# Kernel tuning notes

Measured on AMD Instinct MI355X. Metric: run time of the kernel, lower is better.

The kernel has to match this reference:

```python
import jax, jax.numpy as jnp
import numpy as np

INPUT_SIZE, HIDDEN, OUT = 2, 32, 1

def setup_inputs() -> dict:
    key = jax.random.key(0)
    ks = jax.random.split(key, 8)
    B, T = 2048, 512
    s_ih = 1.0 / np.sqrt(HIDDEN)
    return {
        "x": jax.random.normal(ks[0], (B, T, INPUT_SIZE), dtype=jnp.float32),
        "W_ih": jax.random.uniform(ks[1], (4 * HIDDEN, INPUT_SIZE), minval=-s_ih, maxval=s_ih, dtype=jnp.float32),
        "W_hh": jax.random.uniform(ks[2], (4 * HIDDEN, HIDDEN), minval=-s_ih, maxval=s_ih, dtype=jnp.float32),
        "b_ih": jax.random.uniform(ks[3], (4 * HIDDEN,), minval=-s_ih, maxval=s_ih, dtype=jnp.float32),
        "b_hh": jax.random.uniform(ks[4], (4 * HIDDEN,), minval=-s_ih, maxval=s_ih, dtype=jnp.float32),
        "W_fc": jax.random.uniform(ks[5], (OUT, HIDDEN), minval=-s_ih, maxval=s_ih, dtype=jnp.float32),
        "b_fc": jax.random.uniform(ks[6], (OUT,), minval=-s_ih, maxval=s_ih, dtype=jnp.float32),
    }

def _lstm(x, W_ih, W_hh, b_ih, b_hh):
    # x: [B, T, I]; PyTorch gate order: i, f, g, o
    B, T, _ = x.shape
    H = W_hh.shape[1]
    # precompute input projections for all timesteps: [T, B, 4H]
    xp = jnp.einsum('bti,gi->tbg', x, W_ih) + (b_ih + b_hh)

    def step(carry, xp_t):
        h, c = carry
        gates = xp_t + h @ W_hh.T  # [B, 4H]
        i, f, g, o = jnp.split(gates, 4, axis=-1)
        i = jax.nn.sigmoid(i)
        f = jax.nn.sigmoid(f)
        g = jnp.tanh(g)
        o = jax.nn.sigmoid(o)
        c = f * c + i * g
        h = o * jnp.tanh(c)
        return (h, c), h

    h0 = jnp.zeros((B, H), dtype=x.dtype)
    c0 = jnp.zeros((B, H), dtype=x.dtype)
    _, hs = jax.lax.scan(step, (h0, c0), xp)  # hs: [T, B, H]
    return jnp.transpose(hs, (1, 0, 2))  # [B, T, H]

def reference(x, W_ih, W_hh, b_ih, b_hh, W_fc, b_fc):
    lstm_out = _lstm(x, W_ih, W_hh, b_ih, b_hh)  # [B, T, H]
    return lstm_out @ W_fc.T + b_fc  # [B, T, OUT]
```

## Files before the change

### kernel.cpp

```cpp
#include <hip/hip_runtime.h>


#define BB 2048
#define TT 512
#define HH 32
#define CHUNK 32
#define ROWH 40
#define WSH (2 * CHUNK * ROWH + 8)

#define LOG2E 1.44269504088896340736f

typedef float v2f __attribute__((ext_vector_type(2)));
typedef float v4f __attribute__((ext_vector_type(4)));
typedef unsigned int v4u __attribute__((ext_vector_type(4)));
typedef _Float16 h2 __attribute__((ext_vector_type(2)));

__device__ __forceinline__ float sigm2(float xs) {
    return __builtin_amdgcn_rcpf(1.0f + __builtin_amdgcn_exp2f(-xs));
}

__device__ __forceinline__ h2 u2h(unsigned int u) {
    return __builtin_bit_cast(h2, u);
}

#if defined(__has_builtin)
#if __has_builtin(__builtin_amdgcn_fdot2)
#define FDOT2(a, b, c) __builtin_amdgcn_fdot2((a), (b), (c), false)
#endif
#endif
#ifndef FDOT2
#define FDOT2(a, b, c) fmaf((float)(a).y, (float)(b).y, \
                            fmaf((float)(a).x, (float)(b).x, (c)))
#endif

__global__ __launch_bounds__(256, 1) void lstm_fused_kernel(
    const float* __restrict__ x,
    const float* __restrict__ W_ih,
    const float* __restrict__ W_hh,
    const float* __restrict__ b_ih,
    const float* __restrict__ b_hh,
    const float* __restrict__ W_fc,
    const float* __restrict__ b_fc,
    float* __restrict__ out)
{
    __shared__ __align__(16) _Float16 lds_h[4][WSH];

    const int lane = threadIdx.x & 63;
    const int wv   = threadIdx.x >> 6;
    const int j    = lane & 31;
    const bool low = (lane < 32);
    const int b    = blockIdx.x * 8 + wv * 2 + (low ? 0 : 1);

    const int ri = j, rf = HH + j, rg = 2 * HH + j, ro = 3 * HH + j;
    const float si = LOG2E;
    const float sg = 2.0f * LOG2E;

    const v2f wihI = ((const v2f*)W_ih)[ri] * si;
    const v2f wihF = ((const v2f*)W_ih)[rf] * si;
    const v2f wihG = ((const v2f*)W_ih)[rg] * sg;
    const v2f wihO = ((const v2f*)W_ih)[ro] * si;
    const float bI = (b_ih[ri] + b_hh[ri]) * si;
    const float bF = (b_ih[rf] + b_hh[rf]) * si;
    const float bG = (b_ih[rg] + b_hh[rg]) * sg;
    const float bO = (b_ih[ro] + b_hh[ro]) * si;

    h2 wI[16], wF[16], wG[16], wO[16];
    #pragma unroll
    for (int k = 0; k < 16; ++k) {
        v2f a;
        a = ((const v2f*)(W_hh + ri * HH))[k] * si;
        wI[k] = (h2){(_Float16)a.x, (_Float16)a.y};
        a = ((const v2f*)(W_hh + rf * HH))[k] * si;
        wF[k] = (h2){(_Float16)a.x, (_Float16)a.y};
        a = ((const v2f*)(W_hh + rg * HH))[k] * sg;
        wG[k] = (h2){(_Float16)a.x, (_Float16)a.y};
        a = ((const v2f*)(W_hh + ro * HH))[k] * si;
        wO[k] = (h2){(_Float16)a.x, (_Float16)a.y};
    }

    h2 wfc2[16];
    #pragma unroll
    for (int k = 0; k < 16; ++k) {
        v2f a = ((const v2f*)W_fc)[k];
        wfc2[k] = (h2){(_Float16)a.x, (_Float16)a.y};
    }
    const float bfc = b_fc[0];

    float c = 0.0f;

    _Float16* hb = &lds_h[wv][low ? 0 : CHUNK * ROWH];
    _Float16* wr = hb + j;

    hb[(CHUNK - 1) * ROWH + j] = (_Float16)0.0f;

    v4u hq[4];
    {
        const v4u* rq = (const v4u*)(hb + (CHUNK - 1) * ROWH);
        #pragma unroll
        for (int q = 0; q < 4; ++q) hq[q] = rq[q];
    }

    const float* xb = x + (size_t)b * (TT * 2);
    float* outp = out + (size_t)b * TT + j;

    v4f xq0 = *(const v4f*)(xb);
    v4f xq1 = *(const v4f*)(xb + 4);

    #pragma unroll 1
    for (int ch = 0; ch < TT / CHUNK; ++ch) {
        #pragma unroll 1
        for (int uu = 0; uu < CHUNK; uu += 4) {
            const int t = ch * CHUNK + uu;
            const float* xnx = (t + 4 < TT) ? (xb + (t + 4) * 2) : xb;
            v4f nxq0 = *(const v4f*)(xnx);
            v4f nxq1 = *(const v4f*)(xnx + 4);

            #pragma unroll
            for (int s = 0; s < 4; ++s) {
                v2f xt;
                if      (s == 0) xt = (v2f){xq0.x, xq0.y};
                else if (s == 1) xt = (v2f){xq0.z, xq0.w};
                else if (s == 2) xt = (v2f){xq1.x, xq1.y};
                else             xt = (v2f){xq1.z, xq1.w};

                float aI0 = fmaf(xt.y, wihI.y, fmaf(xt.x, wihI.x, bI));
                float aF0 = fmaf(xt.y, wihF.y, fmaf(xt.x, wihF.x, bF));
                float aG0 = fmaf(xt.y, wihG.y, fmaf(xt.x, wihG.x, bG));
                float aO0 = fmaf(xt.y, wihO.y, fmaf(xt.x, wihO.x, bO));
                float aI1, aF1, aG1, aO1;

                #pragma unroll
                for (int k = 0; k < 16; ++k) {
                    h2 hp = u2h(hq[k >> 2][k & 3]);
                    if (k < 8) {
                        aI0 = FDOT2(hp, wI[k], aI0);
                        aF0 = FDOT2(hp, wF[k], aF0);
                        aG0 = FDOT2(hp, wG[k], aG0);
                        aO0 = FDOT2(hp, wO[k], aO0);
                    } else if (k == 8) {
                        aI1 = FDOT2(hp, wI[k], 0.0f);
                        aF1 = FDOT2(hp, wF[k], 0.0f);
                        aG1 = FDOT2(hp, wG[k], 0.0f);
                        aO1 = FDOT2(hp, wO[k], 0.0f);
                    } else {
                        aI1 = FDOT2(hp, wI[k], aI1);
                        aF1 = FDOT2(hp, wF[k], aF1);
                        aG1 = FDOT2(hp, wG[k], aG1);
                        aO1 = FDOT2(hp, wO[k], aO1);
                    }
                }
                float gi = aI0 + aI1;
                float gf = aF0 + aF1;
                float gg = aG0 + aG1;
                float go = aO0 + aO1;

                float iv = sigm2(gi);
                float fv = sigm2(gf);
                float ov = sigm2(go);
                float gv = fmaf(4.0f * LOG2E, sigm2(gg), -2.0f * LOG2E);

                c = fmaf(fv, c, iv * gv);

                float rr   = sigm2(c);
                float hnew = fmaf(ov + ov, rr, -ov);

                *wr = (_Float16)hnew;
                {
                    const v4u* rq = (const v4u*)(wr - j);
                    #pragma unroll
                    for (int q = 0; q < 4; ++q) hq[q] = rq[q];
                }
                wr += ROWH;
            }
            xq0 = nxq0; xq1 = nxq1;
        }

        wr -= CHUNK * ROWH;

        {
            const v4u* fr = (const v4u*)(hb + j * ROWH);
            v4u f[4];
            #pragma unroll
            for (int q = 0; q < 4; ++q) f[q] = fr[q];
            float acc = bfc;
            #pragma unroll
            for (int k = 0; k < 16; ++k)
                acc = FDOT2(u2h(f[k >> 2][k & 3]), wfc2[k], acc);
            *outp = acc;
            outp += CHUNK;
        }
    }
}

extern "C" void kernel_launch(void* const* d_in, const int* in_sizes, int n_in,
                              void* d_out, int out_size, void* d_ws, size_t ws_size,
                              hipStream_t stream) {
    const float* x    = (const float*)d_in[0];
    const float* W_ih = (const float*)d_in[1];
    const float* W_hh = (const float*)d_in[2];
    const float* b_ih = (const float*)d_in[3];
    const float* b_hh = (const float*)d_in[4];
    const float* W_fc = (const float*)d_in[5];
    const float* b_fc = (const float*)d_in[6];
    float* out = (float*)d_out;

    dim3 grid(BB / 8);
    dim3 block(256);
    lstm_fused_kernel<<<grid, block, 0, stream>>>(x, W_ih, W_hh, b_ih, b_hh,
                                                  W_fc, b_fc, out);
}
```

Measured before the change: 194.1 us.

## Exchange hidden state via permlane32 swap and DPP rotations instead of LDS

Replaces the per-step LDS write and 64-byte readback of the hidden vector with an in-register exchange. A permlane32_swap pairs the two halves, then a tree of DPP row rotations builds all 16 packed h pairs. W_hh weights are permuted to match the rotated lane order through an LDS-staged copy, and the FC head now reads fp32 h rows with a padded stride. This takes LDS latency off the serial recurrence, at the cost of about 15 dependent DPP moves per step and more setup work.

```diff
diff --git a/kernel.cpp b/kernel.cpp
--- a/kernel.cpp
+++ b/kernel.cpp
@@ -5,14 +5,13 @@
 #define TT 512
 #define HH 32
 #define CHUNK 32
-#define ROWH 40
-#define WSH (2 * CHUNK * ROWH + 8)
+#define ROWF 33
 
 #define LOG2E 1.44269504088896340736f
 
 typedef float v2f __attribute__((ext_vector_type(2)));
 typedef float v4f __attribute__((ext_vector_type(4)));
-typedef unsigned int v4u __attribute__((ext_vector_type(4)));
+typedef unsigned int v2u __attribute__((ext_vector_type(2)));
 typedef _Float16 h2 __attribute__((ext_vector_type(2)));
 
 __device__ __forceinline__ float sigm2(float xs) {
@@ -32,6 +31,9 @@
 #define FDOT2(a, b, c) fmaf((float)(a).y, (float)(b).y, \
                             fmaf((float)(a).x, (float)(b).x, (c)))
 #endif
+
+#define DPP_ROR(src, amt) \
+    ((unsigned)__builtin_amdgcn_mov_dpp((int)(src), 0x120 | (amt), 0xf, 0xf, true))
 
 __global__ __launch_bounds__(256, 1) void lstm_fused_kernel(
     const float* __restrict__ x,
@@ -43,17 +45,74 @@
     const float* __restrict__ b_fc,
     float* __restrict__ out)
 {
-    __shared__ __align__(16) _Float16 lds_h[4][WSH];
+    __shared__ float lds_w[128 * HH];
+    __shared__ __align__(16) float lds_h[4][2 * CHUNK * ROWF];
 
     const int lane = threadIdx.x & 63;
     const int wv   = threadIdx.x >> 6;
-    const int j    = lane & 31;
-    const bool low = (lane < 32);
-    const int b    = blockIdx.x * 8 + wv * 2 + (low ? 0 : 1);
+    const bool lo32 = (lane < 32);
+    const int elem = (lane >> 4) & 1;
+    const int j    = (lane & 15) | ((lane >> 1) & 16);
+    const int b    = blockIdx.x * 8 + wv * 2 + elem;
+
+    {
+        const v4f* src = (const v4f*)W_hh;
+        v4f* dst = (v4f*)lds_w;
+        #pragma unroll
+        for (int r = 0; r < (128 * HH / 4) / 256; ++r)
+            dst[r * 256 + threadIdx.x] = src[r * 256 + threadIdx.x];
+    }
+    __syncthreads();
+
+    unsigned P[16];
+    auto exch = [&](float hn) {
+        v2u r = __builtin_amdgcn_permlane32_swap(
+            __float_as_uint(hn), __float_as_uint(hn), false, false);
+        float hx = __uint_as_float(lo32 ? r.y : r.x);
+        h2 pk = {(_Float16)hn, (_Float16)hx};
+        P[0] = __builtin_bit_cast(unsigned, pk);
+        P[1] = DPP_ROR(P[0], 1);
+        P[2] = DPP_ROR(P[0], 2);
+        P[3] = DPP_ROR(P[1], 2);
+        P[4] = DPP_ROR(P[0], 4);
+        P[5] = DPP_ROR(P[1], 4);
+        P[6] = DPP_ROR(P[2], 4);
+        P[7] = DPP_ROR(P[3], 4);
+        P[8]  = DPP_ROR(P[0], 8);
+        P[9]  = DPP_ROR(P[1], 8);
+        P[10] = DPP_ROR(P[2], 8);
+        P[11] = DPP_ROR(P[3], 8);
+        P[12] = DPP_ROR(P[4], 8);
+        P[13] = DPP_ROR(P[5], 8);
+        P[14] = DPP_ROR(P[6], 8);
+        P[15] = DPP_ROR(P[7], 8);
+    };
+
+    exch((float)j);
+    int klo[16], khi[16];
+    #pragma unroll
+    for (int m = 0; m < 16; ++m) {
+        h2 hp = u2h(P[m]);
+        klo[m] = (int)(float)hp.x;
+        khi[m] = (int)(float)hp.y;
+    }
 
     const int ri = j, rf = HH + j, rg = 2 * HH + j, ro = 3 * HH + j;
     const float si = LOG2E;
     const float sg = 2.0f * LOG2E;
+
+    h2 wIp[16], wFp[16], wGp[16], wOp[16];
+    #pragma unroll
+    for (int m = 0; m < 16; ++m) {
+        wIp[m] = (h2){(_Float16)(lds_w[ri * HH + klo[m]] * si),
+                      (_Float16)(lds_w[ri * HH + khi[m]] * si)};
+        wFp[m] = (h2){(_Float16)(lds_w[rf * HH + klo[m]] * si),
+                      (_Float16)(lds_w[rf * HH + khi[m]] * si)};
+        wGp[m] = (h2){(_Float16)(lds_w[rg * HH + klo[m]] * sg),
+                      (_Float16)(lds_w[rg * HH + khi[m]] * sg)};
+        wOp[m] = (h2){(_Float16)(lds_w[ro * HH + klo[m]] * si),
+                      (_Float16)(lds_w[ro * HH + khi[m]] * si)};
+    }
 
     const v2f wihI = ((const v2f*)W_ih)[ri] * si;
     const v2f wihF = ((const v2f*)W_ih)[rf] * si;
@@ -64,41 +123,18 @@
     const float bG = (b_ih[rg] + b_hh[rg]) * sg;
     const float bO = (b_ih[ro] + b_hh[ro]) * si;
 
-    h2 wI[16], wF[16], wG[16], wO[16];
-    #pragma unroll
-    for (int k = 0; k < 16; ++k) {
-        v2f a;
-        a = ((const v2f*)(W_hh + ri * HH))[k] * si;
-        wI[k] = (h2){(_Float16)a.x, (_Float16)a.y};
-        a = ((const v2f*)(W_hh + rf * HH))[k] * si;
-        wF[k] = (h2){(_Float16)a.x, (_Float16)a.y};
-        a = ((const v2f*)(W_hh + rg * HH))[k] * sg;
-        wG[k] = (h2){(_Float16)a.x, (_Float16)a.y};
-        a = ((const v2f*)(W_hh + ro * HH))[k] * si;
-        wO[k] = (h2){(_Float16)a.x, (_Float16)a.y};
-    }
-
-    h2 wfc2[16];
-    #pragma unroll
-    for (int k = 0; k < 16; ++k) {
-        v2f a = ((const v2f*)W_fc)[k];
-        wfc2[k] = (h2){(_Float16)a.x, (_Float16)a.y};
-    }
+    float wfc[HH];
+    #pragma unroll
+    for (int u = 0; u < HH; ++u) wfc[u] = W_fc[u];
     const float bfc = b_fc[0];
 
     float c = 0.0f;
 
-    _Float16* hb = &lds_h[wv][low ? 0 : CHUNK * ROWH];
-    _Float16* wr = hb + j;
-
-    hb[(CHUNK - 1) * ROWH + j] = (_Float16)0.0f;
-
-    v4u hq[4];
-    {
-        const v4u* rq = (const v4u*)(hb + (CHUNK - 1) * ROWH);
-        #pragma unroll
-        for (int q = 0; q < 4; ++q) hq[q] = rq[q];
-    }
+    float* hbE = &lds_h[wv][elem * CHUNK * ROWF];
+    float* wr  = hbE + j;
+
+    #pragma unroll
+    for (int m = 0; m < 16; ++m) P[m] = 0u;
 
     const float* xb = x + (size_t)b * (TT * 2);
     float* outp = out + (size_t)b * TT + j;
@@ -131,22 +167,22 @@
 
                 #pragma unroll
                 for (int k = 0; k < 16; ++k) {
-                    h2 hp = u2h(hq[k >> 2][k & 3]);
+                    h2 hp = u2h(P[k]);
                     if (k < 8) {
-                        aI0 = FDOT2(hp, wI[k], aI0);
-                        aF0 = FDOT2(hp, wF[k], aF0);
-                        aG0 = FDOT2(hp, wG[k], aG0);
-                        aO0 = FDOT2(hp, wO[k], aO0);
+                        aI0 = FDOT2(hp, wIp[k], aI0);
+                        aF0 = FDOT2(hp, wFp[k], aF0);
+                        aG0 = FDOT2(hp, wGp[k], aG0);
+                        aO0 = FDOT2(hp, wOp[k], aO0);
                     } else if (k == 8) {
-                        aI1 = FDOT2(hp, wI[k], 0.0f);
-                        aF1 = FDOT2(hp, wF[k], 0.0f);
-                        aG1 = FDOT2(hp, wG[k], 0.0f);
-                        aO1 = FDOT2(hp, wO[k], 0.0f);
+                        aI1 = FDOT2(hp, wIp[k], 0.0f);
+                        aF1 = FDOT2(hp, wFp[k], 0.0f);
+                        aG1 = FDOT2(hp, wGp[k], 0.0f);
+                        aO1 = FDOT2(hp, wOp[k], 0.0f);
                     } else {
-                        aI1 = FDOT2(hp, wI[k], aI1);
-                        aF1 = FDOT2(hp, wF[k], aF1);
-                        aG1 = FDOT2(hp, wG[k], aG1);
-                        aO1 = FDOT2(hp, wO[k], aO1);
+                        aI1 = FDOT2(hp, wIp[k], aI1);
+                        aF1 = FDOT2(hp, wFp[k], aF1);
+                        aG1 = FDOT2(hp, wGp[k], aG1);
+                        aO1 = FDOT2(hp, wOp[k], aO1);
                     }
                 }
                 float gi = aI0 + aI1;
@@ -164,28 +200,22 @@
                 float rr   = sigm2(c);
                 float hnew = fmaf(ov + ov, rr, -ov);
 
-                *wr = (_Float16)hnew;
-                {
-                    const v4u* rq = (const v4u*)(wr - j);
-                    #pragma unroll
-                    for (int q = 0; q < 4; ++q) hq[q] = rq[q];
-                }
-                wr += ROWH;
+                *wr = hnew;
+                wr += ROWF;
+
+                exch(hnew);
             }
             xq0 = nxq0; xq1 = nxq1;
         }
 
-        wr -= CHUNK * ROWH;
+        wr -= CHUNK * ROWF;
 
         {
-            const v4u* fr = (const v4u*)(hb + j * ROWH);
-            v4u f[4];
-            #pragma unroll
-            for (int q = 0; q < 4; ++q) f[q] = fr[q];
+            const float* frow = hbE + j * ROWF;
             float acc = bfc;
             #pragma unroll
-            for (int k = 0; k < 16; ++k)
-                acc = FDOT2(u2h(f[k >> 2][k & 3]), wfc2[k], acc);
+            for (int u = 0; u < HH; ++u)
+                acc = fmaf(frow[u], wfc[u], acc);
             *outp = acc;
             outp += CHUNK;
         }
```

Result: slower. 199.8 us (+2.9%).
